# Kernel optimization log

Hardware: AMD Instinct MI355X
Metric: run time of the kernel (lower is better)

Reference implementation:

```python
import jax, jax.numpy as jnp
import numpy as np

N_NODES = 50000
N_EDGES = 600000
EPS = 1e-5


def setup_inputs() -> dict:
    key = jax.random.key(0)
    ks = jax.random.split(key, 8)
    return {
        "x": jax.random.normal(ks[0], (N_NODES, 128), dtype=jnp.float32),
        "src": jax.random.randint(ks[1], (N_EDGES,), 0, N_NODES, dtype=jnp.int32),
        "dst": jax.random.randint(ks[2], (N_EDGES,), 0, N_NODES, dtype=jnp.int32),
        "weight": jax.random.uniform(ks[3], (N_EDGES,), dtype=jnp.float32),
        "W1": jax.random.normal(ks[4], (128, 128), dtype=jnp.float32) * 0.05,
        "b1": jnp.zeros((128,), dtype=jnp.float32),
        "gamma1": jnp.ones((128,), dtype=jnp.float32),
        "beta1": jnp.zeros((128,), dtype=jnp.float32),
        "W2": jax.random.normal(ks[5], (128, 64), dtype=jnp.float32) * 0.05,
        "b2": jnp.zeros((64,), dtype=jnp.float32),
        "gamma2": jnp.ones((64,), dtype=jnp.float32),
        "beta2": jnp.zeros((64,), dtype=jnp.float32),
        "W3": jax.random.normal(ks[6], (64, 32), dtype=jnp.float32) * 0.05,
        "b3": jnp.zeros((32,), dtype=jnp.float32),
    }


def _batchnorm(h, gamma, beta):
    # BatchNorm1d in training mode over the node axis (biased variance)
    mean = jnp.mean(h, axis=0)
    var = jnp.mean((h - mean) ** 2, axis=0)
    return gamma * (h - mean) * jax.lax.rsqrt(var + EPS) + beta


def reference(x, src, dst, weight, W1, b1, gamma1, beta1, W2, b2, gamma2, beta2, W3, b3):
    n = x.shape[0]
    # GCNConv: add self-loops with weight 1, symmetric normalization
    loop = jnp.arange(n, dtype=src.dtype)
    src_f = jnp.concatenate([src, loop])  # [E+N]
    dst_f = jnp.concatenate([dst, loop])
    w_f = jnp.concatenate([weight, jnp.ones((n,), dtype=weight.dtype)])
    deg = jax.ops.segment_sum(w_f, dst_f, num_segments=n)  # [N]
    dinv = jnp.where(deg > 0, deg ** -0.5, 0.0)
    norm = dinv[src_f] * w_f * dinv[dst_f]  # [E+N], same for every layer

    def conv(h, W, b):
        h = h @ W  # [N, out]
        msg = norm[:, None] * h[src_f]  # gather + edge scale
        return jax.ops.segment_sum(msg, dst_f, num_segments=n) + b

    h = conv(x, W1, b1)
    h = jax.nn.relu(_batchnorm(h, gamma1, beta1))
    h = conv(h, W2, b2)
    h = jax.nn.relu(_batchnorm(h, gamma2, beta2))
    h = conv(h, W3, b3)  # final BatchNorm is dropped by net[:-1] in encode()
    return h
```

## Files before the change

### kernel.cpp

```cpp
#include <hip/hip_runtime.h>
#include <hip/hip_bf16.h>

#define NN 50000
#define NE 600000
#define SLOTS 48
#define CSTR 16
#define EPT 8
#define FOLD_GRID 32

typedef unsigned short ushortT;
typedef unsigned int uintT;
typedef __attribute__((ext_vector_type(8))) short bf16x8;
typedef __attribute__((ext_vector_type(4))) float f32x4;

__device__ __forceinline__ ushortT f2bfbits(float f) {
    __hip_bfloat16 h = __float2bfloat16(f);
    return *reinterpret_cast<ushortT*>(&h);
}

__device__ __forceinline__ float4 unpack_bf4(uint2 p) {
    float4 r;
    r.x = __uint_as_float(p.x << 16);
    r.y = __uint_as_float(p.x & 0xffff0000u);
    r.z = __uint_as_float(p.y << 16);
    r.w = __uint_as_float(p.y & 0xffff0000u);
    return r;
}

__device__ __forceinline__ int esrc(uintT v) { return (int)(v & 0xFFFFu); }
__device__ __forceinline__ float ew(uintT v) { return __uint_as_float(v & 0xFFFF0000u); }

template <int K, int M>
__device__ __forceinline__ void pack_w_dev(const float* __restrict__ W,
                                           ushortT* __restrict__ Wp, int t) {
    constexpr int KC = K / 32;
    constexpr int CT = M / 16;
    if (t >= CT * KC * 64) return;
    int l = t & 63;
    int q = (t >> 6) % KC;
    int c = t / (64 * KC);
    int m = l & 15, quad = l >> 4;
    alignas(16) ushortT tmp[8];
#pragma unroll
    for (int j = 0; j < 8; ++j)
        tmp[j] = f2bfbits(W[(size_t)(q * 32 + quad * 8 + j) * M + c * 16 + m]);
    *reinterpret_cast<uint4*>(&Wp[(size_t)t * 8]) = *reinterpret_cast<const uint4*>(tmp);
}

__global__ void __launch_bounds__(256) prep_kernel(const float* __restrict__ W1,
                                                   const float* __restrict__ W2,
                                                   const float* __restrict__ W3,
                                                   ushortT* __restrict__ Wp1,
                                                   ushortT* __restrict__ Wp2,
                                                   ushortT* __restrict__ Wp3,
                                                   int* __restrict__ counts,
                                                   float* __restrict__ sums, int n) {
    int b = blockIdx.x, tid = threadIdx.x;
    if (b < 8) {
        pack_w_dev<128, 128>(W1, Wp1, b * 256 + tid);
    } else if (b < 12) {
        pack_w_dev<128, 64>(W2, Wp2, (b - 8) * 256 + tid);
    } else if (b < 13) {
        pack_w_dev<64, 32>(W3, Wp3, (b - 12) * 256 + tid);
    } else {
        int i = (b - 13) * 256 + tid;
        if (i < n) counts[(size_t)i * CSTR] = 0;
        if (b == 13) { sums[tid] = 0.f; sums[256 + tid] = 0.f; }
    }
}

template <typename AT, int K, int M, bool FUSEBN>
__device__ __forceinline__ void gemm_dev(int bid, const AT* __restrict__ A,
                                         const ushortT* __restrict__ Wp,
                                         const float* __restrict__ sums,
                                         const float* __restrict__ gamma,
                                         const float* __restrict__ beta,
                                         ushortT* __restrict__ out, int N) {
    constexpr int KC = K / 32;
    constexpr int CT = M / 16;
    int wave = threadIdx.x >> 6;
    int lane = threadIdx.x & 63;
    int m = lane & 15, quad = lane >> 4;
    int rowbase = bid * 64 + wave * 16;
    int arow = min(rowbase + m, N - 1);

    f32x4 acc[CT] = {};
    const float invN = 1.0f / (float)N;

#pragma unroll
    for (int q = 0; q < KC; ++q) {
        int kb = q * 32 + quad * 8;
        float av[8];
        if constexpr (sizeof(AT) == 4) {
            const float* ap = (const float*)A + (size_t)arow * K + kb;
            float4 lo = *reinterpret_cast<const float4*>(ap);
            float4 hi = *reinterpret_cast<const float4*>(ap + 4);
            av[0] = lo.x; av[1] = lo.y; av[2] = lo.z; av[3] = lo.w;
            av[4] = hi.x; av[5] = hi.y; av[6] = hi.z; av[7] = hi.w;
        } else {
            const ushortT* ap = (const ushortT*)A + (size_t)arow * K + kb;
            uint4 p = *reinterpret_cast<const uint4*>(ap);
            float4 lo = unpack_bf4(make_uint2(p.x, p.y));
            float4 hi = unpack_bf4(make_uint2(p.z, p.w));
            av[0] = lo.x; av[1] = lo.y; av[2] = lo.z; av[3] = lo.w;
            av[4] = hi.x; av[5] = hi.y; av[6] = hi.z; av[7] = hi.w;
        }
        if constexpr (FUSEBN) {
#pragma unroll
            for (int j = 0; j < 8; ++j) {
                int k = kb + j;
                float mean = sums[k] * invN;
                float var = fmaf(-mean, mean, sums[K + k] * invN);
                var = var > 0.f ? var : 0.f;
                float sc = gamma[k] * rsqrtf(var + 1e-5f);
                float sh = fmaf(-mean, sc, beta[k]);
                av[j] = fmaxf(fmaf(av[j], sc, sh), 0.f);
            }
        }
        bf16x8 af;
#pragma unroll
        for (int j = 0; j < 8; ++j) af[j] = (short)f2bfbits(av[j]);
#pragma unroll
        for (int c = 0; c < CT; ++c) {
            bf16x8 bf = *reinterpret_cast<const bf16x8*>(
                &Wp[(((size_t)c * KC + q) * 64 + lane) * 8]);
            acc[c] = __builtin_amdgcn_mfma_f32_16x16x32_bf16(af, bf, acc[c], 0, 0, 0);
        }
    }
#pragma unroll
    for (int c = 0; c < CT; ++c) {
#pragma unroll
        for (int r = 0; r < 4; ++r) {
            int row = rowbase + quad * 4 + r;
            if (row < N) out[(size_t)row * M + c * 16 + m] = f2bfbits(acc[c][r]);
        }
    }
}

__global__ void __launch_bounds__(256) gemm1_fill_kernel(
    const float* __restrict__ x, const ushortT* __restrict__ Wp1,
    ushortT* __restrict__ hlin,
    const int* __restrict__ src, const int* __restrict__ dst, const float* __restrict__ w,
    int* __restrict__ counts, uintT* __restrict__ col_rec, int E, int N, int GB) {
    if ((int)blockIdx.x < GB) {
        gemm_dev<float, 128, 128, false>(blockIdx.x, x, Wp1, nullptr, nullptr, nullptr, hlin, N);
        return;
    }
    int eb = ((int)blockIdx.x - GB) * (256 * EPT) + threadIdx.x;
    int d[EPT];
    uintT rec[EPT];
    int pos[EPT];
#pragma unroll
    for (int k = 0; k < EPT; ++k) {
        int e = eb + k * 256;
        if (e < E) {
            d[k] = dst[e];
            rec[k] = ((uintT)f2bfbits(w[e]) << 16) | (uintT)src[e];
        }
    }
#pragma unroll
    for (int k = 0; k < EPT; ++k) {
        int e = eb + k * 256;
        if (e < E) pos[k] = atomicAdd(&counts[(size_t)d[k] * CSTR], 1);
    }
#pragma unroll
    for (int k = 0; k < EPT; ++k) {
        int e = eb + k * 256;
        if (e < E && pos[k] < SLOTS)
            __builtin_nontemporal_store(rec[k], &col_rec[(size_t)d[k] * SLOTS + pos[k]]);
    }
}

template <typename AT, int K, int M, bool FUSEBN>
__global__ void __launch_bounds__(256) mfma_gemm(const AT* __restrict__ A,
                                                 const ushortT* __restrict__ Wp,
                                                 const float* __restrict__ sums,
                                                 const float* __restrict__ gamma,
                                                 const float* __restrict__ beta,
                                                 ushortT* __restrict__ out, int N) {
    gemm_dev<AT, K, M, FUSEBN>(blockIdx.x, A, Wp, sums, gamma, beta, out, N);
}

__global__ void deg_dinv_kernel(const int* __restrict__ counts, const uintT* __restrict__ col_rec,
                                float* __restrict__ dinv, int* __restrict__ degc, int n) {
    int i = blockIdx.x * 256 + threadIdx.x;
    if (i >= n) return;
    int c = min(counts[(size_t)i * CSTR], SLOTS);
    const uintT* cr = col_rec + (size_t)i * SLOTS;
    float s = 1.0f;
    int j = 0;
    for (; j + 4 <= c; j += 4) {
        uint4 p = *reinterpret_cast<const uint4*>(&cr[j]);
        s += ew(p.x) + ew(p.y) + ew(p.z) + ew(p.w);
    }
    for (; j < c; ++j) s += ew(cr[j]);
    dinv[i] = rsqrtf(s);
    degc[i] = c;
}

template <int TC>
__global__ void __launch_bounds__(256) bn_fold_kernel(const float* __restrict__ partials,
                                                      float* __restrict__ sums, int R) {
    constexpr int C4 = TC / 4;
    constexpr int RL = 256 / C4;
    int tid = threadIdx.x;
    int c4 = tid & (C4 - 1);
    int rl = tid / C4;
    const float4* p4 = reinterpret_cast<const float4*>(partials);
    int stride = FOLD_GRID * RL;
    float4 acc = make_float4(0.f, 0.f, 0.f, 0.f);
    int r = blockIdx.x * RL + rl;
    for (; r + 3 * stride < R; r += 4 * stride) {
        float4 v0 = p4[(size_t)r * C4 + c4];
        float4 v1 = p4[(size_t)(r + stride) * C4 + c4];
        float4 v2 = p4[(size_t)(r + 2 * stride) * C4 + c4];
        float4 v3 = p4[(size_t)(r + 3 * stride) * C4 + c4];
        acc.x += v0.x + v1.x + v2.x + v3.x;
        acc.y += v0.y + v1.y + v2.y + v3.y;
        acc.z += v0.z + v1.z + v2.z + v3.z;
        acc.w += v0.w + v1.w + v2.w + v3.w;
    }
    for (; r < R; r += stride) {
        float4 v = p4[(size_t)r * C4 + c4];
        acc.x += v.x; acc.y += v.y; acc.z += v.z; acc.w += v.w;
    }
    __shared__ float4 sm[256];
    sm[tid] = acc;
    __syncthreads();
    if (rl == 0) {
#pragma unroll
        for (int k = 1; k < RL; ++k) {
            float4 v = sm[k * C4 + c4];
            acc.x += v.x; acc.y += v.y; acc.z += v.z; acc.w += v.w;
        }
        unsafeAtomicAdd(&sums[c4 * 4 + 0], acc.x);
        unsafeAtomicAdd(&sums[c4 * 4 + 1], acc.y);
        unsafeAtomicAdd(&sums[c4 * 4 + 2], acc.z);
        unsafeAtomicAdd(&sums[c4 * 4 + 3], acc.w);
    }
}

template <int C, bool OUTBF, bool FUSEN, bool FUSEBNS>
__global__ void __launch_bounds__(256) csr_agg_kernel(const ushortT* __restrict__ hbf,
                                                      const int* __restrict__ degc,
                                                      const uintT* __restrict__ col_rec,
                                                      float* __restrict__ col_nrm,
                                                      const float* __restrict__ dinv,
                                                      const float* __restrict__ bias,
                                                      void* __restrict__ out,
                                                      float* __restrict__ partials, int N) {
    constexpr int C8 = C / 8;
    constexpr int NPB = 256 / C8;
    int tid = threadIdx.x;
    int idx = blockIdx.x * 256 + tid;
    int node = idx / C8;
    int c8 = tid & (C8 - 1);
    int nl = tid / C8;
    bool valid = node < N;
    if constexpr (!FUSEN && !FUSEBNS) {
        if (!valid) return;
    }
    int nodec = valid ? node : N - 1;

    __shared__ uintT s_rec[FUSEN ? NPB : 1][FUSEN ? SLOTS : 1];
    __shared__ float s_nrm[FUSEN ? NPB : 1][FUSEN ? SLOTS : 1];

    int cnt = valid ? min(degc[nodec], SLOTS) : 0;
    float di = dinv[nodec];

    if constexpr (FUSEN) {
        for (int j = c8; j < cnt; j += C8) {
            uintT r = col_rec[(size_t)node * SLOTS + j];
            float nr = di * ew(r) * dinv[esrc(r)];
            s_rec[nl][j] = r;
            s_nrm[nl][j] = nr;
            col_nrm[(size_t)node * SLOTS + j] = nr;
        }
        __syncthreads();
    }

    const uint4* h8 = reinterpret_cast<const uint4*>(hbf);
    float sl = di * di;
    uint4 hp = h8[valid ? idx : 0];
    float4 hlo = unpack_bf4(make_uint2(hp.x, hp.y));
    float4 hhi = unpack_bf4(make_uint2(hp.z, hp.w));
    float4 blo = *reinterpret_cast<const float4*>(&bias[8 * c8]);
    float4 bhi = *reinterpret_cast<const float4*>(&bias[8 * c8 + 4]);
    float4 alo, ahi;
    alo.x = fmaf(sl, hlo.x, blo.x); alo.y = fmaf(sl, hlo.y, blo.y);
    alo.z = fmaf(sl, hlo.z, blo.z); alo.w = fmaf(sl, hlo.w, blo.w);
    ahi.x = fmaf(sl, hhi.x, bhi.x); ahi.y = fmaf(sl, hhi.y, bhi.y);
    ahi.z = fmaf(sl, hhi.z, bhi.z); ahi.w = fmaf(sl, hhi.w, bhi.w);

    const uintT* crp;
    const float* cnp;
    if constexpr (FUSEN) {
        crp = &s_rec[nl][0];
        cnp = &s_nrm[nl][0];
    } else {
        crp = col_rec + (size_t)nodec * SLOTS;
        cnp = col_nrm + (size_t)nodec * SLOTS;
    }

#define ACC_EDGE(RC, NRM)                                               \
    {                                                                   \
        uint4 p = h8[(size_t)esrc(RC) * C8 + c8];                       \
        float4 lo = unpack_bf4(make_uint2(p.x, p.y));                   \
        float4 hi = unpack_bf4(make_uint2(p.z, p.w));                   \
        alo.x = fmaf(NRM, lo.x, alo.x); alo.y = fmaf(NRM, lo.y, alo.y); \
        alo.z = fmaf(NRM, lo.z, alo.z); alo.w = fmaf(NRM, lo.w, alo.w); \
        ahi.x = fmaf(NRM, hi.x, ahi.x); ahi.y = fmaf(NRM, hi.y, ahi.y); \
        ahi.z = fmaf(NRM, hi.z, ahi.z); ahi.w = fmaf(NRM, hi.w, ahi.w); \
    }

    int j = 0;
    for (; j + 4 <= cnt; j += 4) {
        uint4 rv = *reinterpret_cast<const uint4*>(crp + j);
        float4 nv = *reinterpret_cast<const float4*>(cnp + j);
        ACC_EDGE(rv.x, nv.x);
        ACC_EDGE(rv.y, nv.y);
        ACC_EDGE(rv.z, nv.z);
        ACC_EDGE(rv.w, nv.w);
    }
    for (; j < cnt; ++j) {
        uintT rr = crp[j];
        float nn = cnp[j];
        ACC_EDGE(rr, nn);
    }
#undef ACC_EDGE

    if (valid) {
        if constexpr (OUTBF) {
            alignas(16) ushortT tmp[8];
            tmp[0] = f2bfbits(alo.x); tmp[1] = f2bfbits(alo.y);
            tmp[2] = f2bfbits(alo.z); tmp[3] = f2bfbits(alo.w);
            tmp[4] = f2bfbits(ahi.x); tmp[5] = f2bfbits(ahi.y);
            tmp[6] = f2bfbits(ahi.z); tmp[7] = f2bfbits(ahi.w);
            reinterpret_cast<uint4*>(out)[idx] = *reinterpret_cast<const uint4*>(tmp);
        } else {
            float4* o4 = reinterpret_cast<float4*>(out);
            o4[idx * 2] = alo;
            o4[idx * 2 + 1] = ahi;
        }
    }

    if constexpr (FUSEBNS) {
        float s1[8], s2[8];
        float v[8] = {alo.x, alo.y, alo.z, alo.w, ahi.x, ahi.y, ahi.z, ahi.w};
#pragma unroll
        for (int q = 0; q < 8; ++q) {
            float val = valid ? v[q] : 0.f;
            s1[q] = val;
            s2[q] = val * val;
        }
#pragma unroll
        for (int off = 32; off >= C8; off >>= 1) {
#pragma unroll
            for (int q = 0; q < 8; ++q) {
                s1[q] += __shfl_down(s1[q], off);
                s2[q] += __shfl_down(s2[q], off);
            }
        }
        __shared__ float ps1[4][C8][8], ps2[4][C8][8];
        int lane = tid & 63, wv = tid >> 6;
        if (lane < C8) {
#pragma unroll
            for (int q = 0; q < 8; ++q) { ps1[wv][lane][q] = s1[q]; ps2[wv][lane][q] = s2[q]; }
        }
        __syncthreads();
        if (tid < C8) {
            float a4[8], b4[8];
#pragma unroll
            for (int q = 0; q < 8; ++q) {
                a4[q] = ps1[0][tid][q] + ps1[1][tid][q] + ps1[2][tid][q] + ps1[3][tid][q];
                b4[q] = ps2[0][tid][q] + ps2[1][tid][q] + ps2[2][tid][q] + ps2[3][tid][q];
            }
            float* pr = partials + (size_t)blockIdx.x * (2 * C);
            *reinterpret_cast<float4*>(&pr[tid * 8 + 0]) =
                make_float4(a4[0], a4[1], a4[2], a4[3]);
            *reinterpret_cast<float4*>(&pr[tid * 8 + 4]) =
                make_float4(a4[4], a4[5], a4[6], a4[7]);
            *reinterpret_cast<float4*>(&pr[C + tid * 8 + 0]) =
                make_float4(b4[0], b4[1], b4[2], b4[3]);
            *reinterpret_cast<float4*>(&pr[C + tid * 8 + 4]) =
                make_float4(b4[4], b4[5], b4[6], b4[7]);
        }
    }
}

extern "C" void kernel_launch(void* const* d_in, const int* in_sizes, int n_in,
                              void* d_out, int out_size, void* d_ws, size_t ws_size,
                              hipStream_t stream) {
    const float* x      = (const float*)d_in[0];
    const int*   src    = (const int*)d_in[1];
    const int*   dst    = (const int*)d_in[2];
    const float* weight = (const float*)d_in[3];
    const float* W1     = (const float*)d_in[4];
    const float* b1     = (const float*)d_in[5];
    const float* gamma1 = (const float*)d_in[6];
    const float* beta1  = (const float*)d_in[7];
    const float* W2     = (const float*)d_in[8];
    const float* b2     = (const float*)d_in[9];
    const float* gamma2 = (const float*)d_in[10];
    const float* beta2  = (const float*)d_in[11];
    const float* W3     = (const float*)d_in[12];
    const float* b3     = (const float*)d_in[13];
    float* out = (float*)d_out;

    const int N = NN, E = NE;

    char* ws = (char*)d_ws;
    size_t off = 0;
    auto alloc = [&](size_t bytes) {
        size_t r = off;
        off += (bytes + 255) & ~(size_t)255;
        return r;
    };
    float*   dinv     = (float*)(ws + alloc((size_t)N * 4));
    int*     degc     = (int*)(ws + alloc((size_t)N * 4));
    int*     counts   = (int*)(ws + alloc((size_t)N * CSTR * 4));
    uintT*   col_rec  = (uintT*)(ws + alloc((size_t)N * SLOTS * 4));
    float*   col_nrm  = (float*)(ws + alloc((size_t)N * SLOTS * 4));
    ushortT* hlin_bf  = (ushortT*)(ws + alloc((size_t)N * 128 * 2));
    ushortT* hagg_bf  = (ushortT*)(ws + alloc((size_t)N * 128 * 2));
    ushortT* Wp1      = (ushortT*)(ws + alloc(128 * 128 * 2));
    ushortT* Wp2      = (ushortT*)(ws + alloc(128 * 64 * 2));
    ushortT* Wp3      = (ushortT*)(ws + alloc(64 * 32 * 2));
    float*   sums     = (float*)(ws + alloc(512 * 4));
    float*   sumsA    = sums;
    float*   sumsB    = sums + 256;

    dim3 blk(256);
    auto grd = [](long long n) { return dim3((unsigned)((n + 255) / 256)); };
    const int GB = (N + 63) / 64;
    const int DB = (N + 255) / 256;
    const int FB = (E + 256 * EPT - 1) / (256 * EPT);
    const int AGG1B = (int)(((long long)N * 16 + 255) / 256);
    const int AGG2B = (int)(((long long)N * 8 + 255) / 256);

    float* partials = (float*)(ws + alloc((size_t)AGG1B * 256 * 4));

    prep_kernel<<<13 + DB, blk, 0, stream>>>(W1, W2, W3, Wp1, Wp2, Wp3, counts, sums, N);

    gemm1_fill_kernel<<<GB + FB, blk, 0, stream>>>(x, Wp1, hlin_bf,
                                                   src, dst, weight, counts, col_rec, E, N, GB);
    deg_dinv_kernel<<<DB, blk, 0, stream>>>(counts, col_rec, dinv, degc, N);

    ushortT* h1agg = hagg_bf;
    csr_agg_kernel<128, true, true, true><<<AGG1B, blk, 0, stream>>>(
        hlin_bf, degc, col_rec, col_nrm, dinv, b1, h1agg, partials, N);
    bn_fold_kernel<256><<<FOLD_GRID, 256, 0, stream>>>(partials, sumsA, AGG1B);

    ushortT* h2agg = hagg_bf;
    mfma_gemm<ushortT, 128, 64, true><<<GB, blk, 0, stream>>>(
        h1agg, Wp2, sumsA, gamma1, beta1, hlin_bf, N);
    csr_agg_kernel<64, true, false, true><<<AGG2B, blk, 0, stream>>>(
        hlin_bf, degc, col_rec, col_nrm, dinv, b2, h2agg, partials, N);
    bn_fold_kernel<128><<<FOLD_GRID, 256, 0, stream>>>(partials, sumsB, AGG2B);

    mfma_gemm<ushortT, 64, 32, true><<<GB, blk, 0, stream>>>(
        h2agg, Wp3, sumsB, gamma2, beta2, hlin_bf, N);
    csr_agg_kernel<32, false, false, false><<<grd((long long)N * 4), blk, 0, stream>>>(
        hlin_bf, degc, col_rec, col_nrm, dinv, b3, out, nullptr, N);
}
```

Baseline: 230.9 us.

## Split each node's edge list across wave lanes and reduce with shuffles

The CSR aggregation kernel is restructured so that each wavefront processes a few nodes sequentially. Within a node, its edge list is split across EL lane groups, which each gather a partial sum, and the partials are combined with shuffle reductions. The aim is more memory-level parallelism per node and less load imbalance from variable degree. BN statistics are now accumulated per node inside the loop, and the fill kernel's EPT is halved with the atomic and store merged into one loop. The cost is extra shuffle work and sequential per-wave node loops, which may lower the achievable parallelism.

```diff
diff --git a/kernel.cpp b/kernel.cpp
--- a/kernel.cpp
+++ b/kernel.cpp
@@ -5,7 +5,7 @@
 #define NE 600000
 #define SLOTS 48
 #define CSTR 16
-#define EPT 8
+#define EPT 4
 #define FOLD_GRID 32
 
 typedef unsigned short ushortT;
@@ -149,7 +149,6 @@
     int eb = ((int)blockIdx.x - GB) * (256 * EPT) + threadIdx.x;
     int d[EPT];
     uintT rec[EPT];
-    int pos[EPT];
 #pragma unroll
     for (int k = 0; k < EPT; ++k) {
         int e = eb + k * 256;
@@ -161,13 +160,11 @@
 #pragma unroll
     for (int k = 0; k < EPT; ++k) {
         int e = eb + k * 256;
-        if (e < E) pos[k] = atomicAdd(&counts[(size_t)d[k] * CSTR], 1);
-    }
-#pragma unroll
-    for (int k = 0; k < EPT; ++k) {
-        int e = eb + k * 256;
-        if (e < E && pos[k] < SLOTS)
-            __builtin_nontemporal_store(rec[k], &col_rec[(size_t)d[k] * SLOTS + pos[k]]);
+        if (e < E) {
+            int pos = atomicAdd(&counts[(size_t)d[k] * CSTR], 1);
+            if (pos < SLOTS)
+                __builtin_nontemporal_store(rec[k], &col_rec[(size_t)d[k] * SLOTS + pos]);
+        }
     }
 }
 
@@ -250,119 +247,131 @@
                                                       void* __restrict__ out,
                                                       float* __restrict__ partials, int N) {
     constexpr int C8 = C / 8;
+    constexpr int EL = 64 / C8;
     constexpr int NPB = 256 / C8;
     int tid = threadIdx.x;
-    int idx = blockIdx.x * 256 + tid;
-    int node = idx / C8;
-    int c8 = tid & (C8 - 1);
-    int nl = tid / C8;
-    bool valid = node < N;
-    if constexpr (!FUSEN && !FUSEBNS) {
-        if (!valid) return;
-    }
-    int nodec = valid ? node : N - 1;
+    int lane = tid & 63, wv = tid >> 6;
+    int c8 = lane & (C8 - 1);
+    int el = lane / C8;
+    int nb0 = blockIdx.x * NPB;
 
     __shared__ uintT s_rec[FUSEN ? NPB : 1][FUSEN ? SLOTS : 1];
     __shared__ float s_nrm[FUSEN ? NPB : 1][FUSEN ? SLOTS : 1];
 
-    int cnt = valid ? min(degc[nodec], SLOTS) : 0;
-    float di = dinv[nodec];
-
     if constexpr (FUSEN) {
-        for (int j = c8; j < cnt; j += C8) {
-            uintT r = col_rec[(size_t)node * SLOTS + j];
-            float nr = di * ew(r) * dinv[esrc(r)];
-            s_rec[nl][j] = r;
-            s_nrm[nl][j] = nr;
-            col_nrm[(size_t)node * SLOTS + j] = nr;
+        int nlS = tid / C8;
+        int nodeS = nb0 + nlS;
+        bool vS = nodeS < N;
+        int cS = vS ? min(degc[nodeS], SLOTS) : 0;
+        float diS = dinv[vS ? nodeS : 0];
+        for (int j = c8; j < cS; j += C8) {
+            uintT r = col_rec[(size_t)nodeS * SLOTS + j];
+            float nr = diS * ew(r) * dinv[esrc(r)];
+            s_rec[nlS][j] = r;
+            s_nrm[nlS][j] = nr;
+            col_nrm[(size_t)nodeS * SLOTS + j] = nr;
         }
         __syncthreads();
     }
 
     const uint4* h8 = reinterpret_cast<const uint4*>(hbf);
-    float sl = di * di;
-    uint4 hp = h8[valid ? idx : 0];
-    float4 hlo = unpack_bf4(make_uint2(hp.x, hp.y));
-    float4 hhi = unpack_bf4(make_uint2(hp.z, hp.w));
     float4 blo = *reinterpret_cast<const float4*>(&bias[8 * c8]);
     float4 bhi = *reinterpret_cast<const float4*>(&bias[8 * c8 + 4]);
-    float4 alo, ahi;
-    alo.x = fmaf(sl, hlo.x, blo.x); alo.y = fmaf(sl, hlo.y, blo.y);
-    alo.z = fmaf(sl, hlo.z, blo.z); alo.w = fmaf(sl, hlo.w, blo.w);
-    ahi.x = fmaf(sl, hhi.x, bhi.x); ahi.y = fmaf(sl, hhi.y, bhi.y);
-    ahi.z = fmaf(sl, hhi.z, bhi.z); ahi.w = fmaf(sl, hhi.w, bhi.w);
-
-    const uintT* crp;
-    const float* cnp;
-    if constexpr (FUSEN) {
-        crp = &s_rec[nl][0];
-        cnp = &s_nrm[nl][0];
-    } else {
-        crp = col_rec + (size_t)nodec * SLOTS;
-        cnp = col_nrm + (size_t)nodec * SLOTS;
-    }
-
-#define ACC_EDGE(RC, NRM)                                               \
+    float s1[8] = {}, s2[8] = {};
+
+#define ACC_P(P, NRM)                                                   \
     {                                                                   \
-        uint4 p = h8[(size_t)esrc(RC) * C8 + c8];                       \
-        float4 lo = unpack_bf4(make_uint2(p.x, p.y));                   \
-        float4 hi = unpack_bf4(make_uint2(p.z, p.w));                   \
+        float4 lo = unpack_bf4(make_uint2((P).x, (P).y));               \
+        float4 hi = unpack_bf4(make_uint2((P).z, (P).w));               \
         alo.x = fmaf(NRM, lo.x, alo.x); alo.y = fmaf(NRM, lo.y, alo.y); \
         alo.z = fmaf(NRM, lo.z, alo.z); alo.w = fmaf(NRM, lo.w, alo.w); \
         ahi.x = fmaf(NRM, hi.x, ahi.x); ahi.y = fmaf(NRM, hi.y, ahi.y); \
         ahi.z = fmaf(NRM, hi.z, ahi.z); ahi.w = fmaf(NRM, hi.w, ahi.w); \
     }
 
-    int j = 0;
-    for (; j + 4 <= cnt; j += 4) {
-        uint4 rv = *reinterpret_cast<const uint4*>(crp + j);
-        float4 nv = *reinterpret_cast<const float4*>(cnp + j);
-        ACC_EDGE(rv.x, nv.x);
-        ACC_EDGE(rv.y, nv.y);
-        ACC_EDGE(rv.z, nv.z);
-        ACC_EDGE(rv.w, nv.w);
-    }
-    for (; j < cnt; ++j) {
-        uintT rr = crp[j];
-        float nn = cnp[j];
-        ACC_EDGE(rr, nn);
-    }
-#undef ACC_EDGE
-
-    if (valid) {
-        if constexpr (OUTBF) {
-            alignas(16) ushortT tmp[8];
-            tmp[0] = f2bfbits(alo.x); tmp[1] = f2bfbits(alo.y);
-            tmp[2] = f2bfbits(alo.z); tmp[3] = f2bfbits(alo.w);
-            tmp[4] = f2bfbits(ahi.x); tmp[5] = f2bfbits(ahi.y);
-            tmp[6] = f2bfbits(ahi.z); tmp[7] = f2bfbits(ahi.w);
-            reinterpret_cast<uint4*>(out)[idx] = *reinterpret_cast<const uint4*>(tmp);
+#pragma unroll
+    for (int n = 0; n < EL; ++n) {
+        int nl = wv * EL + n;
+        int node = nb0 + nl;
+        bool valid = node < N;
+        int nodec = valid ? node : N - 1;
+        int cnt = valid ? min(degc[nodec], SLOTS) : 0;
+
+        const uintT* crp;
+        const float* cnp;
+        if constexpr (FUSEN) {
+            crp = &s_rec[nl][0];
+            cnp = &s_nrm[nl][0];
         } else {
-            float4* o4 = reinterpret_cast<float4*>(out);
-            o4[idx * 2] = alo;
-            o4[idx * 2 + 1] = ahi;
-        }
-    }
+            crp = col_rec + (size_t)nodec * SLOTS;
+            cnp = col_nrm + (size_t)nodec * SLOTS;
+        }
+
+        float4 alo = make_float4(0.f, 0.f, 0.f, 0.f);
+        float4 ahi = make_float4(0.f, 0.f, 0.f, 0.f);
+        int j = el;
+        for (; j + EL < cnt; j += 2 * EL) {
+            uintT r0 = crp[j], r1 = crp[j + EL];
+            float m0 = cnp[j], m1 = cnp[j + EL];
+            uint4 p0 = h8[(size_t)esrc(r0) * C8 + c8];
+            uint4 p1 = h8[(size_t)esrc(r1) * C8 + c8];
+            ACC_P(p0, m0);
+            ACC_P(p1, m1);
+        }
+        if (j < cnt) {
+            uintT r0 = crp[j];
+            float m0 = cnp[j];
+            uint4 p0 = h8[(size_t)esrc(r0) * C8 + c8];
+            ACC_P(p0, m0);
+        }
+
+#pragma unroll
+        for (int off = 32; off >= C8; off >>= 1) {
+            alo.x += __shfl_down(alo.x, off); alo.y += __shfl_down(alo.y, off);
+            alo.z += __shfl_down(alo.z, off); alo.w += __shfl_down(alo.w, off);
+            ahi.x += __shfl_down(ahi.x, off); ahi.y += __shfl_down(ahi.y, off);
+            ahi.z += __shfl_down(ahi.z, off); ahi.w += __shfl_down(ahi.w, off);
+        }
+
+        if (el == 0 && valid) {
+            float di = dinv[node];
+            float sl = di * di;
+            uint4 hp = h8[(size_t)node * C8 + c8];
+            float4 hlo = unpack_bf4(make_uint2(hp.x, hp.y));
+            float4 hhi = unpack_bf4(make_uint2(hp.z, hp.w));
+            alo.x += fmaf(sl, hlo.x, blo.x); alo.y += fmaf(sl, hlo.y, blo.y);
+            alo.z += fmaf(sl, hlo.z, blo.z); alo.w += fmaf(sl, hlo.w, blo.w);
+            ahi.x += fmaf(sl, hhi.x, bhi.x); ahi.y += fmaf(sl, hhi.y, bhi.y);
+            ahi.z += fmaf(sl, hhi.z, bhi.z); ahi.w += fmaf(sl, hhi.w, bhi.w);
+
+            if constexpr (OUTBF) {
+                alignas(16) ushortT tmp[8];
+                tmp[0] = f2bfbits(alo.x); tmp[1] = f2bfbits(alo.y);
+                tmp[2] = f2bfbits(alo.z); tmp[3] = f2bfbits(alo.w);
+                tmp[4] = f2bfbits(ahi.x); tmp[5] = f2bfbits(ahi.y);
+                tmp[6] = f2bfbits(ahi.z); tmp[7] = f2bfbits(ahi.w);
+                reinterpret_cast<uint4*>(out)[(size_t)node * C8 + c8] =
+                    *reinterpret_cast<const uint4*>(tmp);
+            } else {
+                float4* o4 = reinterpret_cast<float4*>(out);
+                size_t oi = (size_t)node * C8 + c8;
+                o4[oi * 2] = alo;
+                o4[oi * 2 + 1] = ahi;
+            }
+            if constexpr (FUSEBNS) {
+                float v[8] = {alo.x, alo.y, alo.z, alo.w, ahi.x, ahi.y, ahi.z, ahi.w};
+#pragma unroll
+                for (int q = 0; q < 8; ++q) {
+                    s1[q] += v[q];
+                    s2[q] = fmaf(v[q], v[q], s2[q]);
+                }
+            }
+        }
+    }
+#undef ACC_P
 
     if constexpr (FUSEBNS) {
-        float s1[8], s2[8];
-        float v[8] = {alo.x, alo.y, alo.z, alo.w, ahi.x, ahi.y, ahi.z, ahi.w};
-#pragma unroll
-        for (int q = 0; q < 8; ++q) {
-            float val = valid ? v[q] : 0.f;
-            s1[q] = val;
-            s2[q] = val * val;
-        }
-#pragma unroll
-        for (int off = 32; off >= C8; off >>= 1) {
-#pragma unroll
-            for (int q = 0; q < 8; ++q) {
-                s1[q] += __shfl_down(s1[q], off);
-                s2[q] += __shfl_down(s2[q], off);
-            }
-        }
         __shared__ float ps1[4][C8][8], ps2[4][C8][8];
-        int lane = tid & 63, wv = tid >> 6;
         if (lane < C8) {
 #pragma unroll
             for (int q = 0; q < 8; ++q) { ps1[wv][lane][q] = s1[q]; ps2[wv][lane][q] = s2[q]; }
@@ -435,8 +444,9 @@
     const int GB = (N + 63) / 64;
     const int DB = (N + 255) / 256;
     const int FB = (E + 256 * EPT - 1) / (256 * EPT);
-    const int AGG1B = (int)(((long long)N * 16 + 255) / 256);
-    const int AGG2B = (int)(((long long)N * 8 + 255) / 256);
+    const int AGG1B = (N + 15) / 16;
+    const int AGG2B = (N + 31) / 32;
+    const int AGG3B = (N + 63) / 64;
 
     float* partials = (float*)(ws + alloc((size_t)AGG1B * 256 * 4));
 
@@ -460,6 +470,6 @@
 
     mfma_gemm<ushortT, 64, 32, true><<<GB, blk, 0, stream>>>(
         h2agg, Wp3, sumsB, gamma2, beta2, hlin_bf, N);
-    csr_agg_kernel<32, false, false, false><<<grd((long long)N * 4), blk, 0, stream>>>(
+    csr_agg_kernel<32, false, false, false><<<AGG3B, blk, 0, stream>>>(
         hlin_bf, degc, col_rec, col_nrm, dinv, b3, out, nullptr, N);
 }
```

New measurement: 272.6 us. 1.18x slower.
